# Optimization experiments

Hardware: AMD Instinct MI355X
Metric: run time of the kernel (lower is better)

## Reference

```python
import jax, jax.numpy as jnp
import numpy as np

D_MODEL = 512
D_STATE = 64
EPS = 1e-5


def setup_inputs() -> dict:
    key = jax.random.key(0)
    k1, k2, k3, k4 = jax.random.split(key, 4)
    x = jax.random.normal(k1, (8, 4096, D_MODEL), dtype=jnp.float32)
    A = jax.random.normal(k2, (D_STATE, D_STATE), dtype=jnp.float32) * 0.01
    B = jax.random.normal(k3, (D_STATE, D_MODEL), dtype=jnp.float32) * 0.01
    C = jax.random.normal(k4, (D_MODEL, D_STATE), dtype=jnp.float32) * 0.01
    gamma = jnp.ones((D_MODEL,), dtype=jnp.float32)   # LayerNorm weight
    beta = jnp.zeros((D_MODEL,), dtype=jnp.float32)   # LayerNorm bias
    return {"x": x, "A": A, "B": B, "C": C, "gamma": gamma, "beta": beta}


def reference(x, A, B, C, gamma, beta):
    Bsz, L, D = x.shape
    # precompute input projection u_t @ B.T for all timesteps: [B, L, N]
    Bu = jnp.einsum('bld,nd->bln', x, B)

    def step(state, bu_t):
        # state: [B, N]; bu_t: [B, N]
        new_state = state @ A.T + bu_t
        return new_state, new_state

    state0 = jnp.zeros((Bsz, A.shape[0]), dtype=x.dtype)
    # scan over time dim: inputs [L, B, N]
    _, states = jax.lax.scan(step, state0, jnp.swapaxes(Bu, 0, 1))
    # states: [L, B, N] -> y: [B, L, D]
    y = jnp.einsum('lbn,dn->bld', states, C)
    y = jax.nn.gelu(y, approximate=False)  # torch nn.GELU default is exact erf
    # LayerNorm over last dim
    mean = jnp.mean(y, axis=-1, keepdims=True)
    var = jnp.mean(jnp.square(y - mean), axis=-1, keepdims=True)
    return (y - mean) * jax.lax.rsqrt(var + EPS) * gamma + beta
```

## Files before the change

### kernel.cpp

```cpp
#include <hip/hip_runtime.h>
#include <math.h>

#define L_SEQ 4096
#define DM 512
#define NS 64
#define WARM 32
#define CHUNK 64

typedef __attribute__((ext_vector_type(8))) short short8;
typedef __attribute__((ext_vector_type(4))) float f32x4;

__device__ __forceinline__ unsigned short f2bf(float f) {
    unsigned u = __builtin_bit_cast(unsigned, f);
    u += 0x7FFFu + ((u >> 16) & 1u);
    return (unsigned short)(u >> 16);
}

__device__ __forceinline__ void gll16(const void* g, void* l) {
    __builtin_amdgcn_global_load_lds((const __attribute__((address_space(1))) unsigned*)g,
                                     (__attribute__((address_space(3))) unsigned*)l, 16, 0, 0);
}

__global__ __launch_bounds__(256) void k_bu(const float* __restrict__ x,
                                            const float* __restrict__ Bm,
                                            float* __restrict__ Bu) {
    __shared__ __align__(16) unsigned short xs[64 * 64];
    const int tid = threadIdx.x;
    const int w = tid >> 6, l = tid & 63;
    const int lr = l & 15, lk = l >> 4;
    const int row0 = blockIdx.x * 64;

    short8 bfr[16];
    {
        const float* brow = Bm + (size_t)(w * 16 + lr) * DM + lk * 8;
#pragma unroll
        for (int kf = 0; kf < 16; ++kf) {
            float4 p0 = *(const float4*)(brow + kf * 32);
            float4 p1 = *(const float4*)(brow + kf * 32 + 4);
            short8 f;
            f[0] = (short)f2bf(p0.x); f[1] = (short)f2bf(p0.y);
            f[2] = (short)f2bf(p0.z); f[3] = (short)f2bf(p0.w);
            f[4] = (short)f2bf(p1.x); f[5] = (short)f2bf(p1.y);
            f[6] = (short)f2bf(p1.z); f[7] = (short)f2bf(p1.w);
            bfr[kf] = f;
        }
    }

    f32x4 acc[4];
#pragma unroll
    for (int i = 0; i < 4; ++i) acc[i] = (f32x4)0.f;

    const int sr = tid >> 2;
    const int sq = tid & 3;
#pragma unroll
    for (int kt = 0; kt < 8; ++kt) {
        const float* src = x + (size_t)(row0 + sr) * DM + kt * 64 + sq * 16;
#pragma unroll
        for (int j = 0; j < 4; ++j) {
            float4 v = *(const float4*)(src + j * 4);
            int c = sq * 16 + j * 4;
            int byte = sr * 128 + ((c * 2) ^ ((sr & 7) << 4));
            unsigned long long pk = (unsigned long long)f2bf(v.x)
                                  | ((unsigned long long)f2bf(v.y) << 16)
                                  | ((unsigned long long)f2bf(v.z) << 32)
                                  | ((unsigned long long)f2bf(v.w) << 48);
            *(unsigned long long*)((char*)xs + byte) = pk;
        }
        __syncthreads();
#pragma unroll
        for (int kf = 0; kf < 2; ++kf) {
            const int k = kf * 32 + lk * 8;
#pragma unroll
            for (int mt = 0; mt < 4; ++mt) {
                const int row = mt * 16 + lr;
                short8 af = *(const short8*)((const char*)xs +
                             row * 128 + ((k * 2) ^ ((row & 7) << 4)));
                acc[mt] = __builtin_amdgcn_mfma_f32_16x16x32_bf16(
                              af, bfr[kt * 2 + kf], acc[mt], 0, 0, 0);
            }
        }
        __syncthreads();
    }
#pragma unroll
    for (int mt = 0; mt < 4; ++mt)
#pragma unroll
        for (int r = 0; r < 4; ++r)
            Bu[(size_t)(row0 + mt * 16 + lk * 4 + r) * NS + w * 16 + lr] = acc[mt][r];
}

__global__ __launch_bounds__(256) void k_scan(const float* __restrict__ Bu,
                                              const float* __restrict__ A,
                                              const float* __restrict__ Cm,
                                              float* __restrict__ out) {
    __shared__ float A_lds[64 * 65];
    __shared__ __align__(16) float bu_lds[96 * 64];
    __shared__ __align__(16) unsigned short st_bf[64 * 64];
    __shared__ __align__(16) float s_pp[2][64];

    const int tid = threadIdx.x;
    const int w = tid >> 6, l = tid & 63;
    const int lr = l & 15, lk = l >> 4;
    const int c = blockIdx.x, b = blockIdx.y;
    const int cbase = c * CHUNK;
    const int t0 = (cbase >= WARM) ? (cbase - WARM) : 0;
    const int warm = cbase - t0;
    const int steps = warm + CHUNK;

    for (int idx = tid; idx < 4096; idx += 256)
        A_lds[(idx >> 6) * 65 + (idx & 63)] = A[idx];

    {
        const char* src = (const char*)(Bu + ((size_t)b * L_SEQ + t0) * NS);
        char* dst = (char*)bu_lds + ((tid >> 6) << 10);
        const int nissue = steps >> 4;
        for (int i = 0; i < nissue; ++i)
            gll16(src + i * 4096 + tid * 16, dst + i * 4096);
    }
    __syncthreads();

    if (tid < 64) {
        const int n = tid;
        float a_reg[64];
#pragma unroll
        for (int m = 0; m < 64; ++m) a_reg[m] = A_lds[n * 65 + m];
        s_pp[0][n] = 0.f;
        int cur = 0;
        for (int j = 0; j < steps; ++j) {
            const float4* sp = (const float4*)&s_pp[cur][0];
            float a0 = 0.f, a1 = 0.f, a2 = 0.f, a3 = 0.f;
#pragma unroll
            for (int m4 = 0; m4 < 16; ++m4) {
                float4 v = sp[m4];
                a0 += a_reg[4 * m4 + 0] * v.x;
                a1 += a_reg[4 * m4 + 1] * v.y;
                a2 += a_reg[4 * m4 + 2] * v.z;
                a3 += a_reg[4 * m4 + 3] * v.w;
            }
            float s = ((a0 + a1) + (a2 + a3)) + bu_lds[j * 64 + n];
            cur ^= 1;
            s_pp[cur][n] = s;
            int jj = j - warm;
            if (jj >= 0) st_bf[jj * 64 + (n ^ ((jj & 7) << 3))] = f2bf(s);
        }
    }
    __syncthreads();

    short8 sfr[2][4];
#pragma unroll
    for (int kf = 0; kf < 2; ++kf) {
        const int k = kf * 32 + lk * 8;
#pragma unroll
        for (int mt = 0; mt < 4; ++mt) {
            const int t = mt * 16 + lr;
            sfr[kf][mt] = *(const short8*)((const char*)st_bf +
                           t * 128 + ((k * 2) ^ ((t & 7) << 4)));
        }
    }

    const size_t orow0 = (size_t)b * L_SEQ + cbase;
#pragma unroll
    for (int dt = 0; dt < 4; ++dt) {
        short8 cfr[2][2];
#pragma unroll
        for (int nt = 0; nt < 2; ++nt) {
            const int d = dt * 128 + w * 32 + nt * 16 + lr;
            const float* crow = Cm + (size_t)d * NS + lk * 8;
#pragma unroll
            for (int kf = 0; kf < 2; ++kf) {
                float4 p0 = *(const float4*)(crow + kf * 32);
                float4 p1 = *(const float4*)(crow + kf * 32 + 4);
                short8 f;
                f[0] = (short)f2bf(p0.x); f[1] = (short)f2bf(p0.y);
                f[2] = (short)f2bf(p0.z); f[3] = (short)f2bf(p0.w);
                f[4] = (short)f2bf(p1.x); f[5] = (short)f2bf(p1.y);
                f[6] = (short)f2bf(p1.z); f[7] = (short)f2bf(p1.w);
                cfr[nt][kf] = f;
            }
        }
        f32x4 acc[4][2];
#pragma unroll
        for (int mt = 0; mt < 4; ++mt)
#pragma unroll
            for (int nt = 0; nt < 2; ++nt) acc[mt][nt] = (f32x4)0.f;
#pragma unroll
        for (int kf = 0; kf < 2; ++kf)
#pragma unroll
            for (int mt = 0; mt < 4; ++mt)
#pragma unroll
                for (int nt = 0; nt < 2; ++nt)
                    acc[mt][nt] = __builtin_amdgcn_mfma_f32_16x16x32_bf16(
                                      sfr[kf][mt], cfr[nt][kf], acc[mt][nt], 0, 0, 0);
#pragma unroll
        for (int mt = 0; mt < 4; ++mt)
#pragma unroll
            for (int nt = 0; nt < 2; ++nt) {
                const int d = dt * 128 + w * 32 + nt * 16 + lr;
#pragma unroll
                for (int r = 0; r < 4; ++r) {
                    const int t = mt * 16 + lk * 4 + r;
                    float y = acc[mt][nt][r];
                    y = 0.5f * y * (1.f + erff(y * 0.70710678118654752f));
                    out[(orow0 + t) * DM + d] = y;
                }
            }
    }
}

__global__ __launch_bounds__(256) void k_ln(float* __restrict__ out,
                                            const float* __restrict__ gamma,
                                            const float* __restrict__ beta) {
    __shared__ float red[8];
    const size_t row = blockIdx.x;
    float* p = out + row * DM;
    const int tid = threadIdx.x;

    float2 v = ((const float2*)p)[tid];
    float s = v.x + v.y;
    float q = v.x * v.x + v.y * v.y;
#pragma unroll
    for (int off = 32; off; off >>= 1) {
        s += __shfl_down(s, off);
        q += __shfl_down(q, off);
    }
    const int wid = tid >> 6, lane = tid & 63;
    if (lane == 0) { red[wid] = s; red[4 + wid] = q; }
    __syncthreads();
    if (tid == 0) {
        float ts = red[0] + red[1] + red[2] + red[3];
        float tq = red[4] + red[5] + red[6] + red[7];
        float mean = ts * (1.f / 512.f);
        float var = tq * (1.f / 512.f) - mean * mean;
        red[0] = mean;
        red[1] = rsqrtf(var + 1e-5f);
    }
    __syncthreads();
    const float mean = red[0], rstd = red[1];
    float2 g = ((const float2*)gamma)[tid];
    float2 be = ((const float2*)beta)[tid];
    float2 o;
    o.x = (v.x - mean) * rstd * g.x + be.x;
    o.y = (v.y - mean) * rstd * g.y + be.y;
    ((float2*)p)[tid] = o;
}

extern "C" void kernel_launch(void* const* d_in, const int* in_sizes, int n_in,
                              void* d_out, int out_size, void* d_ws, size_t ws_size,
                              hipStream_t stream) {
    const float* x     = (const float*)d_in[0];
    const float* A     = (const float*)d_in[1];
    const float* B     = (const float*)d_in[2];
    const float* Cm    = (const float*)d_in[3];
    const float* gamma = (const float*)d_in[4];
    const float* beta  = (const float*)d_in[5];
    float* out = (float*)d_out;
    float* Bu  = (float*)d_ws;

    k_bu<<<dim3(512), dim3(256), 0, stream>>>(x, B, Bu);
    k_scan<<<dim3(64, 8), dim3(256), 0, stream>>>(Bu, A, Cm, out);
    k_ln<<<dim3(32768), dim3(256), 0, stream>>>(out, gamma, beta);
}
```

Before: 199.9 us.

## Replace serial scan with matrix-power blocked scan and fuse LayerNorm into output GEMM

Adds a kernel that precomputes A^0..A^16 in bf16. The serial 96-step per-chunk recurrence becomes a sum of A^p·Bu terms on MFMA over 16-step blocks, with only 4 serial A^16 steps to carry state between blocks and a correction GEMM afterwards. Bu is stored in bf16, and LayerNorm is fused into the scan kernel by recomputing the C-projection GEMM and GELU in a second pass, which removes the separate k_ln read/write of the output. This trades extra MFMA work, a larger LDS footprint and lower precision (bf16 powers and states) for less serial latency and less memory traffic.

```diff
diff --git a/kernel.cpp b/kernel.cpp
--- a/kernel.cpp
+++ b/kernel.cpp
@@ -4,8 +4,6 @@
 #define L_SEQ 4096
 #define DM 512
 #define NS 64
-#define WARM 32
-#define CHUNK 64
 
 typedef __attribute__((ext_vector_type(8))) short short8;
 typedef __attribute__((ext_vector_type(4))) float f32x4;
@@ -15,15 +13,67 @@
     u += 0x7FFFu + ((u >> 16) & 1u);
     return (unsigned short)(u >> 16);
 }
-
+__device__ __forceinline__ float gelu_f(float y) {
+    return 0.5f * y * (1.f + erff(y * 0.70710678118654752f));
+}
 __device__ __forceinline__ void gll16(const void* g, void* l) {
     __builtin_amdgcn_global_load_lds((const __attribute__((address_space(1))) unsigned*)g,
                                      (__attribute__((address_space(3))) unsigned*)l, 16, 0, 0);
 }
 
+__global__ __launch_bounds__(256) void k_pow(const float* __restrict__ A,
+                                             unsigned short* __restrict__ pows_bf,
+                                             float* __restrict__ A16f) {
+    __shared__ __align__(16) unsigned short cur[2][64 * 64];
+    __shared__ __align__(16) unsigned short At[64 * 64];
+    const int tid = threadIdx.x, w = tid >> 6, l = tid & 63;
+    const int lr = l & 15, lk = l >> 4;
+    for (int idx = tid; idx < 4096; idx += 256) {
+        float a = A[idx];
+        unsigned short bv = f2bf(a);
+        cur[1][idx] = bv;
+        At[(idx & 63) * 64 + (idx >> 6)] = bv;
+        pows_bf[4096 + idx] = bv;
+        pows_bf[idx] = ((idx >> 6) == (idx & 63)) ? (unsigned short)0x3F80 : (unsigned short)0;
+    }
+    __syncthreads();
+    short8 bfr[4][2];
+#pragma unroll
+    for (int nt = 0; nt < 4; ++nt)
+#pragma unroll
+        for (int kf = 0; kf < 2; ++kf)
+            bfr[nt][kf] = *(const short8*)(At + (nt * 16 + lr) * 64 + kf * 32 + lk * 8);
+    for (int p = 2; p <= 16; ++p) {
+        const int src = (p - 1) & 1, dst = p & 1;
+        short8 af[2];
+#pragma unroll
+        for (int kf = 0; kf < 2; ++kf)
+            af[kf] = *(const short8*)(cur[src] + (w * 16 + lr) * 64 + kf * 32 + lk * 8);
+        f32x4 acc[4];
+#pragma unroll
+        for (int nt = 0; nt < 4; ++nt) acc[nt] = (f32x4)0.f;
+#pragma unroll
+        for (int kf = 0; kf < 2; ++kf)
+#pragma unroll
+            for (int nt = 0; nt < 4; ++nt)
+                acc[nt] = __builtin_amdgcn_mfma_f32_16x16x32_bf16(af[kf], bfr[nt][kf], acc[nt], 0, 0, 0);
+#pragma unroll
+        for (int nt = 0; nt < 4; ++nt)
+#pragma unroll
+            for (int r = 0; r < 4; ++r) {
+                int i = w * 16 + lk * 4 + r, j = nt * 16 + lr;
+                unsigned short bv = f2bf(acc[nt][r]);
+                cur[dst][i * 64 + j] = bv;
+                pows_bf[p * 4096 + i * 64 + j] = bv;
+                if (p == 16) A16f[i * 64 + j] = acc[nt][r];
+            }
+        __syncthreads();
+    }
+}
+
 __global__ __launch_bounds__(256) void k_bu(const float* __restrict__ x,
                                             const float* __restrict__ Bm,
-                                            float* __restrict__ Bu) {
+                                            unsigned short* __restrict__ Bu_bf) {
     __shared__ __align__(16) unsigned short xs[64 * 64];
     const int tid = threadIdx.x;
     const int w = tid >> 6, l = tid & 63;
@@ -45,13 +95,11 @@
             bfr[kf] = f;
         }
     }
-
     f32x4 acc[4];
 #pragma unroll
     for (int i = 0; i < 4; ++i) acc[i] = (f32x4)0.f;
 
-    const int sr = tid >> 2;
-    const int sq = tid & 3;
+    const int sr = tid >> 2, sq = tid & 3;
 #pragma unroll
     for (int kt = 0; kt < 8; ++kt) {
         const float* src = x + (size_t)(row0 + sr) * DM + kt * 64 + sq * 16;
@@ -73,10 +121,8 @@
 #pragma unroll
             for (int mt = 0; mt < 4; ++mt) {
                 const int row = mt * 16 + lr;
-                short8 af = *(const short8*)((const char*)xs +
-                             row * 128 + ((k * 2) ^ ((row & 7) << 4)));
-                acc[mt] = __builtin_amdgcn_mfma_f32_16x16x32_bf16(
-                              af, bfr[kt * 2 + kf], acc[mt], 0, 0, 0);
+                short8 af = *(const short8*)((const char*)xs + row * 128 + ((k * 2) ^ ((row & 7) << 4)));
+                acc[mt] = __builtin_amdgcn_mfma_f32_16x16x32_bf16(af, bfr[kt * 2 + kf], acc[mt], 0, 0, 0);
             }
         }
         __syncthreads();
@@ -84,80 +130,193 @@
 #pragma unroll
     for (int mt = 0; mt < 4; ++mt)
 #pragma unroll
-        for (int r = 0; r < 4; ++r)
-            Bu[(size_t)(row0 + mt * 16 + lk * 4 + r) * NS + w * 16 + lr] = acc[mt][r];
-}
-
-__global__ __launch_bounds__(256) void k_scan(const float* __restrict__ Bu,
-                                              const float* __restrict__ A,
+        for (int r = 0; r < 4; ++r) {
+            int tp = mt * 16 + lk * 4 + r, n = w * 16 + lr;
+            xs[tp * 64 + (n ^ ((tp & 7) << 3))] = f2bf(acc[mt][r]);
+        }
+    __syncthreads();
+#pragma unroll
+    for (int q = 0; q < 2; ++q) {
+        int slot = tid + q * 256;
+        *(float4*)((char*)Bu_bf + (size_t)row0 * 128 + slot * 16) =
+            *(const float4*)((const char*)xs + slot * 16);
+    }
+}
+
+__global__ __launch_bounds__(256) void k_mega(const unsigned short* __restrict__ Bu_bf,
+                                              const unsigned short* __restrict__ pows_bf,
+                                              const float* __restrict__ A16f,
                                               const float* __restrict__ Cm,
-                                              float* __restrict__ out) {
-    __shared__ float A_lds[64 * 65];
-    __shared__ __align__(16) float bu_lds[96 * 64];
+                                              const float* __restrict__ gamma,
+                                              const float* __restrict__ beta,
+                                              float* __restrict__ outp) {
+    __shared__ __align__(16) unsigned short bu_lds[96 * 64];
     __shared__ __align__(16) unsigned short st_bf[64 * 64];
+    __shared__ __align__(16) float G_lds[4][16][64];
+    __shared__ __align__(16) unsigned short Sb_bf[16 * 64];
+    __shared__ __align__(16) float W_lds[6][64];
     __shared__ __align__(16) float s_pp[2][64];
+    __shared__ float red1[64][4];
+    __shared__ float red2[64][4];
+    __shared__ float mv[64][2];
+    __shared__ __align__(16) float y_slice[64][128];
 
     const int tid = threadIdx.x;
     const int w = tid >> 6, l = tid & 63;
     const int lr = l & 15, lk = l >> 4;
     const int c = blockIdx.x, b = blockIdx.y;
-    const int cbase = c * CHUNK;
-    const int t0 = (cbase >= WARM) ? (cbase - WARM) : 0;
-    const int warm = cbase - t0;
-    const int steps = warm + CHUNK;
-
-    for (int idx = tid; idx < 4096; idx += 256)
-        A_lds[(idx >> 6) * 65 + (idx & 63)] = A[idx];
+    const int cbase = c * 64;
+    const long t0 = (long)cbase - 32;
+
+    for (int idx = tid; idx < 1024; idx += 256) Sb_bf[idx] = 0;
 
     {
-        const char* src = (const char*)(Bu + ((size_t)b * L_SEQ + t0) * NS);
-        char* dst = (char*)bu_lds + ((tid >> 6) << 10);
-        const int nissue = steps >> 4;
-        for (int i = 0; i < nissue; ++i)
-            gll16(src + i * 4096 + tid * 16, dst + i * 4096);
+        const char* src = (const char*)Bu_bf + ((long)b * L_SEQ + t0) * 128;
+        char* dstb = (char*)bu_lds + ((tid >> 6) << 10);
+        if (c == 0) {
+            float4 z = make_float4(0.f, 0.f, 0.f, 0.f);
+            *(float4*)((char*)bu_lds + tid * 16) = z;
+            for (int j = 1; j < 3; ++j) gll16(src + j * 4096 + tid * 16, dstb + j * 4096);
+        } else {
+            for (int j = 0; j < 3; ++j) gll16(src + j * 4096 + tid * 16, dstb + j * 4096);
+        }
+    }
+    __syncthreads();
+
+    const int nT = (w < 2) ? 2 : 1;
+    f32x4 P0[4], P1[4];
+#pragma unroll
+    for (int mt = 0; mt < 4; ++mt) { P0[mt] = (f32x4)0.f; P1[mt] = (f32x4)0.f; }
+    const short8 zfrag = {};
+    for (int p = 0; p < 16; ++p) {
+        short8 af[4][2];
+#pragma unroll
+        for (int mt = 0; mt < 4; ++mt)
+#pragma unroll
+            for (int kf = 0; kf < 2; ++kf)
+                af[mt][kf] = *(const short8*)(pows_bf + p * 4096 + (mt * 16 + lr) * 64 + kf * 32 + lk * 8);
+        const bool maskz = (lr < p);
+        {
+            int jrow = w * 16 + lr - p; int jc = jrow < 0 ? 0 : jrow;
+#pragma unroll
+            for (int kf = 0; kf < 2; ++kf) {
+                short8 bf = *(const short8*)((const char*)bu_lds + jc * 128 + ((kf * 64 + lk * 16) ^ ((jc & 7) << 4)));
+                if (maskz) bf = zfrag;
+#pragma unroll
+                for (int mt = 0; mt < 4; ++mt)
+                    P0[mt] = __builtin_amdgcn_mfma_f32_16x16x32_bf16(af[mt][kf], bf, P0[mt], 0, 0, 0);
+            }
+        }
+        if (nT == 2) {
+            int jrow = (w + 4) * 16 + lr - p; int jc = jrow < 0 ? 0 : jrow;
+#pragma unroll
+            for (int kf = 0; kf < 2; ++kf) {
+                short8 bf = *(const short8*)((const char*)bu_lds + jc * 128 + ((kf * 64 + lk * 16) ^ ((jc & 7) << 4)));
+                if (maskz) bf = zfrag;
+#pragma unroll
+                for (int mt = 0; mt < 4; ++mt)
+                    P1[mt] = __builtin_amdgcn_mfma_f32_16x16x32_bf16(af[mt][kf], bf, P1[mt], 0, 0, 0);
+            }
+        }
+    }
+    if (lr == 15) {
+#pragma unroll
+        for (int mt = 0; mt < 4; ++mt) *(float4*)&W_lds[w][mt * 16 + lk * 4] = *(float4*)&P0[mt];
+        if (nT == 2) {
+#pragma unroll
+            for (int mt = 0; mt < 4; ++mt) *(float4*)&W_lds[w + 4][mt * 16 + lk * 4] = *(float4*)&P1[mt];
+        }
     }
     __syncthreads();
 
     if (tid < 64) {
         const int n = tid;
-        float a_reg[64];
-#pragma unroll
-        for (int m = 0; m < 64; ++m) a_reg[m] = A_lds[n * 65 + m];
-        s_pp[0][n] = 0.f;
-        int cur = 0;
-        for (int j = 0; j < steps; ++j) {
-            const float4* sp = (const float4*)&s_pp[cur][0];
+        float a16r[64];
+#pragma unroll
+        for (int q = 0; q < 16; ++q) {
+            float4 t4 = *(const float4*)(A16f + n * 64 + q * 4);
+            a16r[q * 4] = t4.x; a16r[q * 4 + 1] = t4.y; a16r[q * 4 + 2] = t4.z; a16r[q * 4 + 3] = t4.w;
+        }
+        float s = W_lds[0][n];
+#pragma unroll
+        for (int g = 1; g <= 4; ++g) {
+            s_pp[g & 1][n] = s;
+            const float4* sp = (const float4*)&s_pp[g & 1][0];
             float a0 = 0.f, a1 = 0.f, a2 = 0.f, a3 = 0.f;
 #pragma unroll
             for (int m4 = 0; m4 < 16; ++m4) {
                 float4 v = sp[m4];
-                a0 += a_reg[4 * m4 + 0] * v.x;
-                a1 += a_reg[4 * m4 + 1] * v.y;
-                a2 += a_reg[4 * m4 + 2] * v.z;
-                a3 += a_reg[4 * m4 + 3] * v.w;
-            }
-            float s = ((a0 + a1) + (a2 + a3)) + bu_lds[j * 64 + n];
-            cur ^= 1;
-            s_pp[cur][n] = s;
-            int jj = j - warm;
-            if (jj >= 0) st_bf[jj * 64 + (n ^ ((jj & 7) << 3))] = f2bf(s);
-        }
+                a0 += a16r[4 * m4 + 0] * v.x;
+                a1 += a16r[4 * m4 + 1] * v.y;
+                a2 += a16r[4 * m4 + 2] * v.z;
+                a3 += a16r[4 * m4 + 3] * v.w;
+            }
+            s = ((a0 + a1) + (a2 + a3)) + W_lds[g][n];
+            Sb_bf[(g - 1) * 64 + n] = f2bf(s);
+        }
+    }
+    __syncthreads();
+
+    {
+        short8 sb[2];
+#pragma unroll
+        for (int kf = 0; kf < 2; ++kf)
+            sb[kf] = *(const short8*)(Sb_bf + lr * 64 + kf * 32 + lk * 8);
+        for (int i = 0; i < 16; ++i) {
+            const int mtg = w * 16 + i;
+            const int r = mtg >> 2, ms = (mtg & 3) * 16 + lr;
+            f32x4 ga = (f32x4)0.f;
+#pragma unroll
+            for (int kf = 0; kf < 2; ++kf) {
+                short8 af = *(const short8*)(pows_bf + (r + 1) * 4096 + ms * 64 + kf * 32 + lk * 8);
+                ga = __builtin_amdgcn_mfma_f32_16x16x32_bf16(af, sb[kf], ga, 0, 0, 0);
+            }
+            if (lr < 4) *(float4*)&G_lds[lr][r][(mtg & 3) * 16 + lk * 4] = *(float4*)&ga;
+        }
+    }
+    __syncthreads();
+
+    {
+        const int ot = (w < 2) ? (w + 4) : w;
+        const int cc = ot - 2;
+        const int tt = ot * 16 + lr - 32;
+#define MERGE_BODY(PACC)                                                            \
+        {                                                                           \
+            _Pragma("unroll")                                                       \
+            for (int mt = 0; mt < 4; ++mt) {                                        \
+                float4 corr = *(const float4*)&G_lds[cc][lr][mt * 16 + lk * 4];     \
+                float v0 = PACC[mt][0] + corr.x, v1 = PACC[mt][1] + corr.y;         \
+                float v2 = PACC[mt][2] + corr.z, v3 = PACC[mt][3] + corr.w;         \
+                unsigned long long pk = (unsigned long long)f2bf(v0)                \
+                                      | ((unsigned long long)f2bf(v1) << 16)        \
+                                      | ((unsigned long long)f2bf(v2) << 32)        \
+                                      | ((unsigned long long)f2bf(v3) << 48);       \
+                int m0 = mt * 16 + lk * 4;                                          \
+                *(unsigned long long*)((char*)st_bf + tt * 128 +                    \
+                                       ((m0 * 2) ^ ((tt & 7) << 4))) = pk;          \
+            }                                                                       \
+        }
+        if (w < 2) MERGE_BODY(P1) else MERGE_BODY(P0)
+#undef MERGE_BODY
     }
     __syncthreads();
 
     short8 sfr[2][4];
 #pragma unroll
-    for (int kf = 0; kf < 2; ++kf) {
-        const int k = kf * 32 + lk * 8;
+    for (int kf = 0; kf < 2; ++kf)
 #pragma unroll
         for (int mt = 0; mt < 4; ++mt) {
-            const int t = mt * 16 + lr;
-            sfr[kf][mt] = *(const short8*)((const char*)st_bf +
-                           t * 128 + ((k * 2) ^ ((t & 7) << 4)));
-        }
-    }
+            int t = mt * 16 + lr;
+            sfr[kf][mt] = *(const short8*)((const char*)st_bf + t * 128 + (((kf * 32 + lk * 8) * 2) ^ ((t & 7) << 4)));
+        }
 
     const size_t orow0 = (size_t)b * L_SEQ + cbase;
+    float s1[4][4], s2[4][4];
+#pragma unroll
+    for (int mt = 0; mt < 4; ++mt)
+#pragma unroll
+        for (int r = 0; r < 4; ++r) { s1[mt][r] = 0.f; s2[mt][r] = 0.f; }
+
 #pragma unroll
     for (int dt = 0; dt < 4; ++dt) {
         short8 cfr[2][2];
@@ -188,59 +347,99 @@
             for (int mt = 0; mt < 4; ++mt)
 #pragma unroll
                 for (int nt = 0; nt < 2; ++nt)
-                    acc[mt][nt] = __builtin_amdgcn_mfma_f32_16x16x32_bf16(
-                                      sfr[kf][mt], cfr[nt][kf], acc[mt][nt], 0, 0, 0);
-#pragma unroll
-        for (int mt = 0; mt < 4; ++mt)
-#pragma unroll
-            for (int nt = 0; nt < 2; ++nt) {
-                const int d = dt * 128 + w * 32 + nt * 16 + lr;
+                    acc[mt][nt] = __builtin_amdgcn_mfma_f32_16x16x32_bf16(sfr[kf][mt], cfr[nt][kf], acc[mt][nt], 0, 0, 0);
+#pragma unroll
+        for (int mt = 0; mt < 4; ++mt)
+#pragma unroll
+            for (int nt = 0; nt < 2; ++nt)
 #pragma unroll
                 for (int r = 0; r < 4; ++r) {
-                    const int t = mt * 16 + lk * 4 + r;
-                    float y = acc[mt][nt][r];
-                    y = 0.5f * y * (1.f + erff(y * 0.70710678118654752f));
-                    out[(orow0 + t) * DM + d] = y;
+                    float yv = gelu_f(acc[mt][nt][r]);
+                    s1[mt][r] += yv; s2[mt][r] += yv * yv;
                 }
-            }
-    }
-}
-
-__global__ __launch_bounds__(256) void k_ln(float* __restrict__ out,
-                                            const float* __restrict__ gamma,
-                                            const float* __restrict__ beta) {
-    __shared__ float red[8];
-    const size_t row = blockIdx.x;
-    float* p = out + row * DM;
-    const int tid = threadIdx.x;
-
-    float2 v = ((const float2*)p)[tid];
-    float s = v.x + v.y;
-    float q = v.x * v.x + v.y * v.y;
-#pragma unroll
-    for (int off = 32; off; off >>= 1) {
-        s += __shfl_down(s, off);
-        q += __shfl_down(q, off);
-    }
-    const int wid = tid >> 6, lane = tid & 63;
-    if (lane == 0) { red[wid] = s; red[4 + wid] = q; }
-    __syncthreads();
-    if (tid == 0) {
-        float ts = red[0] + red[1] + red[2] + red[3];
-        float tq = red[4] + red[5] + red[6] + red[7];
+    }
+#pragma unroll
+    for (int mask = 1; mask < 16; mask <<= 1)
+#pragma unroll
+        for (int mt = 0; mt < 4; ++mt)
+#pragma unroll
+            for (int r = 0; r < 4; ++r) {
+                s1[mt][r] += __shfl_xor(s1[mt][r], mask);
+                s2[mt][r] += __shfl_xor(s2[mt][r], mask);
+            }
+    if (lr == 0) {
+#pragma unroll
+        for (int mt = 0; mt < 4; ++mt)
+#pragma unroll
+            for (int r = 0; r < 4; ++r) {
+                int tt = mt * 16 + lk * 4 + r;
+                red1[tt][w] = s1[mt][r]; red2[tt][w] = s2[mt][r];
+            }
+    }
+    __syncthreads();
+    if (tid < 64) {
+        float ts = red1[tid][0] + red1[tid][1] + red1[tid][2] + red1[tid][3];
+        float tq = red2[tid][0] + red2[tid][1] + red2[tid][2] + red2[tid][3];
         float mean = ts * (1.f / 512.f);
         float var = tq * (1.f / 512.f) - mean * mean;
-        red[0] = mean;
-        red[1] = rsqrtf(var + 1e-5f);
-    }
-    __syncthreads();
-    const float mean = red[0], rstd = red[1];
-    float2 g = ((const float2*)gamma)[tid];
-    float2 be = ((const float2*)beta)[tid];
-    float2 o;
-    o.x = (v.x - mean) * rstd * g.x + be.x;
-    o.y = (v.y - mean) * rstd * g.y + be.y;
-    ((float2*)p)[tid] = o;
+        mv[tid][0] = mean;
+        mv[tid][1] = rsqrtf(var + 1e-5f);
+    }
+    __syncthreads();
+
+#pragma unroll
+    for (int dt = 0; dt < 4; ++dt) {
+        short8 cfr[2][2];
+#pragma unroll
+        for (int nt = 0; nt < 2; ++nt) {
+            const int d = dt * 128 + w * 32 + nt * 16 + lr;
+            const float* crow = Cm + (size_t)d * NS + lk * 8;
+#pragma unroll
+            for (int kf = 0; kf < 2; ++kf) {
+                float4 p0 = *(const float4*)(crow + kf * 32);
+                float4 p1 = *(const float4*)(crow + kf * 32 + 4);
+                short8 f;
+                f[0] = (short)f2bf(p0.x); f[1] = (short)f2bf(p0.y);
+                f[2] = (short)f2bf(p0.z); f[3] = (short)f2bf(p0.w);
+                f[4] = (short)f2bf(p1.x); f[5] = (short)f2bf(p1.y);
+                f[6] = (short)f2bf(p1.z); f[7] = (short)f2bf(p1.w);
+                cfr[nt][kf] = f;
+            }
+        }
+        f32x4 acc[4][2];
+#pragma unroll
+        for (int mt = 0; mt < 4; ++mt)
+#pragma unroll
+            for (int nt = 0; nt < 2; ++nt) acc[mt][nt] = (f32x4)0.f;
+#pragma unroll
+        for (int kf = 0; kf < 2; ++kf)
+#pragma unroll
+            for (int mt = 0; mt < 4; ++mt)
+#pragma unroll
+                for (int nt = 0; nt < 2; ++nt)
+                    acc[mt][nt] = __builtin_amdgcn_mfma_f32_16x16x32_bf16(sfr[kf][mt], cfr[nt][kf], acc[mt][nt], 0, 0, 0);
+#pragma unroll
+        for (int nt = 0; nt < 2; ++nt) {
+            const int d = dt * 128 + w * 32 + nt * 16 + lr;
+            const float gm = gamma[d], bt = beta[d];
+#pragma unroll
+            for (int mt = 0; mt < 4; ++mt)
+#pragma unroll
+                for (int r = 0; r < 4; ++r) {
+                    int tt = mt * 16 + lk * 4 + r;
+                    float yv = gelu_f(acc[mt][nt][r]);
+                    y_slice[tt][w * 32 + nt * 16 + lr] = (yv - mv[tt][0]) * mv[tt][1] * gm + bt;
+                }
+        }
+        __syncthreads();
+#pragma unroll
+        for (int q = 0; q < 8; ++q) {
+            int slot = tid + q * 256;
+            int row = slot >> 5, c4 = (slot & 31) << 2;
+            *(float4*)&outp[(orow0 + row) * DM + dt * 128 + c4] = *(const float4*)&y_slice[row][c4];
+        }
+        __syncthreads();
+    }
 }
 
 extern "C" void kernel_launch(void* const* d_in, const int* in_sizes, int n_in,
@@ -253,9 +452,12 @@
     const float* gamma = (const float*)d_in[4];
     const float* beta  = (const float*)d_in[5];
     float* out = (float*)d_out;
-    float* Bu  = (float*)d_ws;
-
-    k_bu<<<dim3(512), dim3(256), 0, stream>>>(x, B, Bu);
-    k_scan<<<dim3(64, 8), dim3(256), 0, stream>>>(Bu, A, Cm, out);
-    k_ln<<<dim3(32768), dim3(256), 0, stream>>>(out, gamma, beta);
-}
+
+    unsigned short* Bu_bf   = (unsigned short*)d_ws;
+    unsigned short* pows_bf = (unsigned short*)((char*)d_ws + (4u << 20));
+    float*          A16f    = (float*)((char*)d_ws + (4u << 20) + 139264);
+
+    k_pow<<<dim3(1), dim3(256), 0, stream>>>(A, pows_bf, A16f);
+    k_bu<<<dim3(512), dim3(256), 0, stream>>>(x, B, Bu_bf);
+    k_mega<<<dim3(64, 8), dim3(256), 0, stream>>>(Bu_bf, pows_bf, A16f, Cm, gamma, beta, out);
+}
```

Result: slower. 262.9 us (+31.5%).
